# Kernel optimization log

Measured on AMD Instinct MI355X. Metric: run time of the kernel, lower is better.

## Reference

```python
import jax, jax.numpy as jnp
import numpy as np

H = W = 1536
DT = 0.02
FAST_DT, SLOW_DT = 1.0, 0.2
EPS_FAST, EPS_SLOW = 0.06, 0.02
F2S, S2F = 0.04, 0.02


def setup_inputs() -> dict:
    key = jax.random.key(0)
    k1, k2, k3 = jax.random.split(key, 3)
    phi = jax.random.normal(k1, (1, 10, H, W), jnp.float32)
    sensory_map = jax.random.normal(k2, (1, 1, H, W), jnp.float32)
    gamma = jnp.array([0.2, 0.15, 0.1, 0.18, 0.12, 0.13, 0.14, 0.16, 0.11, 0.1], jnp.float32)
    alpha = jnp.array([0.3, 0.25, 0.22, 0.18, 0.2, 0.15, 0.19, 0.24, 0.17, 0.16], jnp.float32)
    mix_w = jax.random.normal(k3, (10, 10), jnp.float32) * 0.1  # 1x1 conv weight, no bias
    return {"phi": phi, "sensory_map": sensory_map, "gamma": gamma, "alpha": alpha, "mix_w": mix_w}


def _lap(x):
    # periodic 5-point Laplacian via rolls on the last two (spatial) dims
    return (jnp.roll(x, 1, -2) + jnp.roll(x, -1, -2)
            + jnp.roll(x, 1, -1) + jnp.roll(x, -1, -1) - 4.0 * x)


def _step(phi, sensory_map, gamma, alpha, mix_w):
    lap = _lap(phi)
    bilap = _lap(lap)
    g, a, p = gamma, alpha, phi
    ch = [
        -g[0] * lap[:, 0] - a[0] * p[:, 0] ** 3 + 0.12 * bilap[:, 0],
        -g[1] * lap[:, 1] + 0.15 * jnp.sin(p[:, 1]) + 0.08 * p[:, 1] ** 3,
        -g[2] * lap[:, 2] + 0.2 * p[:, 2] * (1.0 - p[:, 2] ** 2),
        -g[3] * lap[:, 3] - 0.03 * p[:, 3] ** 5 + 0.08 * bilap[:, 3],
        -g[4] * lap[:, 4] + 0.12 * p[:, 4] * jnp.log(jnp.abs(p[:, 4]) + 1e-6) + 0.02 * bilap[:, 4],
        -g[5] * lap[:, 5] + 0.08 * p[:, 5] ** 3 - 0.02 * p[:, 5] ** 5,
        -g[6] * lap[:, 6] + 0.06 * p[:, 6] ** 4 - 0.04 * p[:, 6],
        -g[7] * lap[:, 7] + 0.08 * jnp.sinh(jnp.clip(p[:, 7], -2.0, 2.0)),
        -g[8] * lap[:, 8] + 0.05 * p[:, 8] ** 2 - 0.08 * p[:, 8],
        -g[9] * lap[:, 9] + 0.02 * p[:, 9] ** 6 - 0.04 * p[:, 9] ** 3 + 0.01 * bilap[:, 9],
    ]
    dphi = jnp.stack(ch, axis=1)                                 # [1,10,H,W]
    coupling = jnp.einsum('oc,bchw->bohw', mix_w, phi)            # 1x1 conv, no bias
    fast_mean = phi[:, :5].mean(axis=1, keepdims=True)            # [1,1,H,W]
    slow_mean = phi[:, 5:].mean(axis=1, keepdims=True)
    sd = sensory_map[:, 0]                                        # [1,H,W]
    dphi_f = dphi[:, :5] + EPS_FAST * coupling[:, :5] + S2F * slow_mean
    dphi_s = dphi[:, 5:] + EPS_SLOW * coupling[:, 5:] + F2S * fast_mean
    dphi_f = dphi_f.at[:, 0].add(0.2 * sd).at[:, 4].add(0.08 * jnp.abs(sd))
    dphi_s = dphi_s.at[:, 4].add(0.05 * sd)                       # global channel 9
    phi_next = jnp.concatenate([phi[:, :5] + DT * FAST_DT * dphi_f,
                                phi[:, 5:] + DT * SLOW_DT * dphi_s], axis=1)
    return jnp.clip(phi_next, -4.0, 4.0)


def reference(phi, sensory_map, gamma, alpha, mix_w):
    phi_next = _step(phi, sensory_map, gamma, alpha, mix_w)
    phi1_mean = phi_next[:, 0].mean(axis=(1, 2))
    phi5_mean = phi_next[:, 4].mean(axis=(1, 2))
    field_means = phi_next.mean(axis=(2, 3))
    return phi_next, phi1_mean, phi5_mean, field_means
```

## Files before the change

### kernel.cpp

```cpp
#include <hip/hip_runtime.h>
#include <math.h>

#define HH 1536
#define WW 1536
#define HWSZ (HH*WW)
#define NT 384

__device__ __forceinline__ float4 LD4(const float* __restrict__ p, int row, int t) {
    return reinterpret_cast<const float4*>(p + row)[t];
}

__global__ __launch_bounds__(NT) void step_kernel(
    const float* __restrict__ phi,
    const float* __restrict__ sensory,
    const float* __restrict__ gamma,
    const float* __restrict__ alpha,
    const float* __restrict__ mixw,
    float* __restrict__ out,
    float* __restrict__ sums)
{
    __shared__ float s_mix[100];
    __shared__ float s_g[10];
    __shared__ float s_a0;
    __shared__ float s_red[6][10];

    const int tid = threadIdx.x;
    if (tid < 100) s_mix[tid] = mixw[tid];
    if (tid < 10)  s_g[tid]   = gamma[tid];
    if (tid == 0)  s_a0       = alpha[0];
    __syncthreads();

    const int blk = blockIdx.x;
    const int y = (blk & 7) * 192 + (blk >> 3);

    const int x0 = tid * 4;

    const int ym1 = (y == 0)      ? HH - 1     : y - 1;
    const int yp1 = (y == HH - 1) ? 0          : y + 1;
    const int ym2 = (y < 2)       ? y + HH - 2 : y - 2;
    const int yp2 = (y >= HH - 2) ? y - HH + 2 : y + 2;

    const int r0  = y   * WW;
    const int rm1 = ym1 * WW;
    const int rp1 = yp1 * WW;
    const int rm2 = ym2 * WW;
    const int rp2 = yp2 * WW;

    const int xl1 = (x0 == 0)        ? WW - 1 : x0 - 1;
    const int xl2 = (x0 == 0)        ? WW - 2 : x0 - 2;
    const int xr1 = (x0 + 4 == WW)   ? 0      : x0 + 4;
    const int xr2 = (x0 + 4 == WW)   ? 1      : x0 + 5;

    float pv[10][4];
    float dv[10][4];

    #pragma unroll
    for (int c = 0; c < 10; ++c) {
        const float* pc = phi + (size_t)c * HWSZ;
        const float4 cm = LD4(pc, r0,  tid);
        const float4 nn = LD4(pc, rm1, tid);
        const float4 ss = LD4(pc, rp1, tid);
        const float wl1 = pc[r0 + xl1];
        const float wr1 = pc[r0 + xr1];

        float lap[4];
        lap[0] = nn.x + ss.x + wl1  + cm.y - 4.0f * cm.x;
        lap[1] = nn.y + ss.y + cm.x + cm.z - 4.0f * cm.y;
        lap[2] = nn.z + ss.z + cm.y + cm.w - 4.0f * cm.z;
        lap[3] = nn.w + ss.w + cm.z + wr1  - 4.0f * cm.w;

        float bl[4] = {0.f, 0.f, 0.f, 0.f};
        if (c == 0 || c == 3 || c == 4 || c == 9) {
            const float4 t2n = LD4(pc, rm2, tid);
            const float4 t2s = LD4(pc, rp2, tid);
            const float wl2 = pc[r0  + xl2];
            const float wr2 = pc[r0  + xr2];
            const float nwl = pc[rm1 + xl1];
            const float ner = pc[rm1 + xr1];
            const float swl = pc[rp1 + xl1];
            const float ser = pc[rp1 + xr1];
            bl[0] = 20.0f*cm.x - 8.0f*(nn.x + ss.x + wl1  + cm.y)
                  + 2.0f*(nwl  + nn.y + swl  + ss.y) + (t2n.x + t2s.x + wl2  + cm.z);
            bl[1] = 20.0f*cm.y - 8.0f*(nn.y + ss.y + cm.x + cm.z)
                  + 2.0f*(nn.x + nn.z + ss.x + ss.z) + (t2n.y + t2s.y + wl1  + cm.w);
            bl[2] = 20.0f*cm.z - 8.0f*(nn.z + ss.z + cm.y + cm.w)
                  + 2.0f*(nn.y + nn.w + ss.y + ss.w) + (t2n.z + t2s.z + cm.x + wr1);
            bl[3] = 20.0f*cm.w - 8.0f*(nn.w + ss.w + cm.z + wr1)
                  + 2.0f*(nn.z + ner  + ss.z + ser ) + (t2n.w + t2s.w + cm.y + wr2);
        }

        pv[c][0] = cm.x; pv[c][1] = cm.y; pv[c][2] = cm.z; pv[c][3] = cm.w;

        #pragma unroll
        for (int k = 0; k < 4; ++k) {
            const float pp = pv[c][k];
            const float lv = lap[k];
            const float bv = bl[k];
            float dd;
            switch (c) {
            case 0: dd = -s_g[0]*lv - s_a0*pp*pp*pp + 0.12f*bv; break;
            case 1: dd = -s_g[1]*lv + 0.15f*sinf(pp) + 0.08f*pp*pp*pp; break;
            case 2: dd = -s_g[2]*lv + 0.2f*pp*(1.0f - pp*pp); break;
            case 3: { const float p2 = pp*pp;
                      dd = -s_g[3]*lv - 0.03f*p2*p2*pp + 0.08f*bv; } break;
            case 4: dd = -s_g[4]*lv + 0.12f*pp*logf(fabsf(pp) + 1e-6f) + 0.02f*bv; break;
            case 5: { const float p2 = pp*pp;
                      dd = -s_g[5]*lv + 0.08f*p2*pp - 0.02f*p2*p2*pp; } break;
            case 6: { const float p2 = pp*pp;
                      dd = -s_g[6]*lv + 0.06f*p2*p2 - 0.04f*pp; } break;
            case 7: { const float pc7 = fminf(fmaxf(pp, -2.0f), 2.0f);
                      dd = -s_g[7]*lv + 0.08f*sinhf(pc7); } break;
            case 8: dd = -s_g[8]*lv + 0.05f*pp*pp - 0.08f*pp; break;
            default: { const float p3 = pp*pp*pp;
                       dd = -s_g[9]*lv + 0.02f*p3*p3 - 0.04f*p3 + 0.01f*bv; } break;
            }
            dv[c][k] = dd;
        }
    }

    float fmv[4], smv[4], sdk[4];
    {
        const float4 sd4 = LD4(sensory, r0, tid);
        sdk[0] = sd4.x; sdk[1] = sd4.y; sdk[2] = sd4.z; sdk[3] = sd4.w;
        #pragma unroll
        for (int k = 0; k < 4; ++k) {
            fmv[k] = (pv[0][k] + pv[1][k] + pv[2][k] + pv[3][k] + pv[4][k]) * 0.2f;
            smv[k] = (pv[5][k] + pv[6][k] + pv[7][k] + pv[8][k] + pv[9][k]) * 0.2f;
        }
    }

    const int lane = tid & 63;
    const int wave = tid >> 6;

    #pragma unroll
    for (int o = 0; o < 10; ++o) {
        float pn[4];
        #pragma unroll
        for (int k = 0; k < 4; ++k) {
            float cp = 0.0f;
            #pragma unroll
            for (int c = 0; c < 10; ++c) cp = fmaf(s_mix[o*10 + c], pv[c][k], cp);
            float dd = dv[o][k];
            if (o < 5) {
                dd += 0.06f * cp + 0.02f * smv[k];
                if (o == 0) dd += 0.2f  * sdk[k];
                if (o == 4) dd += 0.08f * fabsf(sdk[k]);
                pn[k] = pv[o][k] + 0.02f * dd;
            } else {
                dd += 0.02f * cp + 0.04f * fmv[k];
                if (o == 9) dd += 0.05f * sdk[k];
                pn[k] = pv[o][k] + 0.004f * dd;
            }
            pn[k] = fminf(fmaxf(pn[k], -4.0f), 4.0f);
        }
        float4 o4; o4.x = pn[0]; o4.y = pn[1]; o4.z = pn[2]; o4.w = pn[3];
        reinterpret_cast<float4*>(out + (size_t)o * HWSZ + r0)[tid] = o4;

        float s = pn[0] + pn[1] + pn[2] + pn[3];
        #pragma unroll
        for (int off = 32; off > 0; off >>= 1) s += __shfl_down(s, off, 64);
        if (lane == 0) s_red[wave][o] = s;
    }

    __syncthreads();
    if (tid < 10) {
        float v = 0.0f;
        #pragma unroll
        for (int w = 0; w < 6; ++w) v += s_red[w][tid];
        atomicAdd(&sums[tid], v);
    }
}

__global__ void finalize_kernel(const float* __restrict__ sums,
                                float* __restrict__ out)
{
    const int t = threadIdx.x;
    const float inv = 1.0f / (float)HWSZ;
    const size_t base = (size_t)10 * HWSZ;
    if (t == 0) out[base]     = sums[0] * inv;
    if (t == 1) out[base + 1] = sums[4] * inv;
    if (t >= 2 && t < 12) out[base + 2 + (t - 2)] = sums[t - 2] * inv;
}

extern "C" void kernel_launch(void* const* d_in, const int* in_sizes, int n_in,
                              void* d_out, int out_size, void* d_ws, size_t ws_size,
                              hipStream_t stream) {
    const float* phi     = (const float*)d_in[0];
    const float* sensory = (const float*)d_in[1];
    const float* gamma   = (const float*)d_in[2];
    const float* alpha   = (const float*)d_in[3];
    const float* mixw    = (const float*)d_in[4];
    float* out = (float*)d_out;
    float* sums = (float*)d_ws;

    hipMemsetAsync(sums, 0, 10 * sizeof(float), stream);

    step_kernel<<<dim3(HH), NT, 0, stream>>>(phi, sensory, gamma, alpha, mixw, out, sums);
    finalize_kernel<<<1, 64, 0, stream>>>(sums, out);
}
```

Before: 240.2 us.

## Fold coupling, means and timestep into premixed weights and use fast intrinsics

Precomputes a combined 10x10 weight matrix that folds the coupling epsilon, the fast/slow channel means and the per-group timestep, so accumulation into the next state happens incrementally per input channel. This removes the separate dphi and phi arrays and the mean computations, which cuts register pressure. It also switches sinf, logf and sinhf to fast intrinsic forms (__sinf, __logf, __expf), trading some accuracy for fewer instructions.

```diff
diff --git a/kernel.cpp b/kernel.cpp
--- a/kernel.cpp
+++ b/kernel.cpp
@@ -19,15 +19,24 @@
     float* __restrict__ out,
     float* __restrict__ sums)
 {
-    __shared__ float s_mix[100];
+    __shared__ float s_wdt[100];
     __shared__ float s_g[10];
     __shared__ float s_a0;
     __shared__ float s_red[6][10];
 
     const int tid = threadIdx.x;
-    if (tid < 100) s_mix[tid] = mixw[tid];
-    if (tid < 10)  s_g[tid]   = gamma[tid];
-    if (tid == 0)  s_a0       = alpha[0];
+    if (tid < 100) {
+        const int o = tid / 10;
+        const int c = tid % 10;
+        const float eps  = (o < 5) ? 0.06f : 0.02f;
+        const float dt_o = (o < 5) ? 0.02f : 0.004f;
+        float w = eps * mixw[tid];
+        if (o < 5 && c >= 5) w += 0.02f * 0.2f;
+        if (o >= 5 && c < 5) w += 0.04f * 0.2f;
+        s_wdt[tid] = dt_o * w;
+    }
+    if (tid < 10)  s_g[tid] = gamma[tid];
+    if (tid == 0)  s_a0     = alpha[0];
     __syncthreads();
 
     const int blk = blockIdx.x;
@@ -51,8 +60,11 @@
     const int xr1 = (x0 + 4 == WW)   ? 0      : x0 + 4;
     const int xr2 = (x0 + 4 == WW)   ? 1      : x0 + 5;
 
-    float pv[10][4];
-    float dv[10][4];
+    float pn[10][4];
+    #pragma unroll
+    for (int o = 0; o < 10; ++o)
+        #pragma unroll
+        for (int k = 0; k < 4; ++k) pn[o][k] = 0.0f;
 
     #pragma unroll
     for (int c = 0; c < 10; ++c) {
@@ -62,6 +74,8 @@
         const float4 ss = LD4(pc, rp1, tid);
         const float wl1 = pc[r0 + xl1];
         const float wr1 = pc[r0 + xr1];
+
+        float pvk[4] = {cm.x, cm.y, cm.z, cm.w};
 
         float lap[4];
         lap[0] = nn.x + ss.x + wl1  + cm.y - 4.0f * cm.x;
@@ -89,43 +103,50 @@
                   + 2.0f*(nn.z + ner  + ss.z + ser ) + (t2n.w + t2s.w + cm.y + wr2);
         }
 
-        pv[c][0] = cm.x; pv[c][1] = cm.y; pv[c][2] = cm.z; pv[c][3] = cm.w;
+        const float dtc = (c < 5) ? 0.02f : 0.004f;
 
         #pragma unroll
         for (int k = 0; k < 4; ++k) {
-            const float pp = pv[c][k];
+            const float pp = pvk[k];
             const float lv = lap[k];
             const float bv = bl[k];
             float dd;
             switch (c) {
             case 0: dd = -s_g[0]*lv - s_a0*pp*pp*pp + 0.12f*bv; break;
-            case 1: dd = -s_g[1]*lv + 0.15f*sinf(pp) + 0.08f*pp*pp*pp; break;
+            case 1: dd = -s_g[1]*lv + 0.15f*__sinf(pp) + 0.08f*pp*pp*pp; break;
             case 2: dd = -s_g[2]*lv + 0.2f*pp*(1.0f - pp*pp); break;
             case 3: { const float p2 = pp*pp;
                       dd = -s_g[3]*lv - 0.03f*p2*p2*pp + 0.08f*bv; } break;
-            case 4: dd = -s_g[4]*lv + 0.12f*pp*logf(fabsf(pp) + 1e-6f) + 0.02f*bv; break;
+            case 4: dd = -s_g[4]*lv + 0.12f*pp*__logf(fabsf(pp) + 1e-6f) + 0.02f*bv; break;
             case 5: { const float p2 = pp*pp;
                       dd = -s_g[5]*lv + 0.08f*p2*pp - 0.02f*p2*p2*pp; } break;
             case 6: { const float p2 = pp*pp;
                       dd = -s_g[6]*lv + 0.06f*p2*p2 - 0.04f*pp; } break;
             case 7: { const float pc7 = fminf(fmaxf(pp, -2.0f), 2.0f);
-                      dd = -s_g[7]*lv + 0.08f*sinhf(pc7); } break;
+                      dd = -s_g[7]*lv + 0.04f*(__expf(pc7) - __expf(-pc7)); } break;
             case 8: dd = -s_g[8]*lv + 0.05f*pp*pp - 0.08f*pp; break;
             default: { const float p3 = pp*pp*pp;
                        dd = -s_g[9]*lv + 0.02f*p3*p3 - 0.04f*p3 + 0.01f*bv; } break;
             }
-            dv[c][k] = dd;
-        }
-    }
-
-    float fmv[4], smv[4], sdk[4];
+            pn[c][k] += pp + dtc * dd;
+        }
+
+        #pragma unroll
+        for (int o = 0; o < 10; ++o) {
+            const float w = s_wdt[o*10 + c];
+            #pragma unroll
+            for (int k = 0; k < 4; ++k) pn[o][k] = fmaf(w, pvk[k], pn[o][k]);
+        }
+    }
+
     {
         const float4 sd4 = LD4(sensory, r0, tid);
-        sdk[0] = sd4.x; sdk[1] = sd4.y; sdk[2] = sd4.z; sdk[3] = sd4.w;
+        const float sdk[4] = {sd4.x, sd4.y, sd4.z, sd4.w};
         #pragma unroll
         for (int k = 0; k < 4; ++k) {
-            fmv[k] = (pv[0][k] + pv[1][k] + pv[2][k] + pv[3][k] + pv[4][k]) * 0.2f;
-            smv[k] = (pv[5][k] + pv[6][k] + pv[7][k] + pv[8][k] + pv[9][k]) * 0.2f;
+            pn[0][k] += 0.02f  * (0.2f  * sdk[k]);
+            pn[4][k] += 0.02f  * (0.08f * fabsf(sdk[k]));
+            pn[9][k] += 0.004f * (0.05f * sdk[k]);
         }
     }
 
@@ -134,29 +155,15 @@
 
     #pragma unroll
     for (int o = 0; o < 10; ++o) {
-        float pn[4];
-        #pragma unroll
-        for (int k = 0; k < 4; ++k) {
-            float cp = 0.0f;
-            #pragma unroll
-            for (int c = 0; c < 10; ++c) cp = fmaf(s_mix[o*10 + c], pv[c][k], cp);
-            float dd = dv[o][k];
-            if (o < 5) {
-                dd += 0.06f * cp + 0.02f * smv[k];
-                if (o == 0) dd += 0.2f  * sdk[k];
-                if (o == 4) dd += 0.08f * fabsf(sdk[k]);
-                pn[k] = pv[o][k] + 0.02f * dd;
-            } else {
-                dd += 0.02f * cp + 0.04f * fmv[k];
-                if (o == 9) dd += 0.05f * sdk[k];
-                pn[k] = pv[o][k] + 0.004f * dd;
-            }
-            pn[k] = fminf(fmaxf(pn[k], -4.0f), 4.0f);
-        }
-        float4 o4; o4.x = pn[0]; o4.y = pn[1]; o4.z = pn[2]; o4.w = pn[3];
+        float4 o4;
+        float* pk = pn[o];
+        o4.x = fminf(fmaxf(pk[0], -4.0f), 4.0f);
+        o4.y = fminf(fmaxf(pk[1], -4.0f), 4.0f);
+        o4.z = fminf(fmaxf(pk[2], -4.0f), 4.0f);
+        o4.w = fminf(fmaxf(pk[3], -4.0f), 4.0f);
         reinterpret_cast<float4*>(out + (size_t)o * HWSZ + r0)[tid] = o4;
 
-        float s = pn[0] + pn[1] + pn[2] + pn[3];
+        float s = o4.x + o4.y + o4.z + o4.w;
         #pragma unroll
         for (int off = 32; off > 0; off >>= 1) s += __shfl_down(s, off, 64);
         if (lane == 0) s_red[wave][o] = s;
```

Result: slower. 279.5 us (+16.3%).
